# Kernel optimization log

Hardware: AMD Instinct MI355X
Metric: run time of the kernel (lower is better)

The kernel has to match this reference:

```python
import jax, jax.numpy as jnp
import numpy as np

B, T, E, H = 2, 2048, 1024, 4
Dk = E // H          # 256 head qk dim
Dv = Dk * 2          # 512 head v dim (expansion_ratio=2)
EPS = 1e-5
ROPE_BASE = 10000.0


def setup_inputs() -> dict:
    key = jax.random.key(0)
    ks = jax.random.split(key, 7)
    s = 0.02  # small init matching xavier gains in reset_parameters
    return {
        "x": jax.random.normal(ks[0], (B, T, E), jnp.float32),
        "Wq": jax.random.normal(ks[1], (E, E), jnp.float32) * s,
        "Wk": jax.random.normal(ks[2], (E, E), jnp.float32) * s,
        "Wv": jax.random.normal(ks[3], (E, 2 * E), jnp.float32) * s,
        "Wg": jax.random.normal(ks[4], (E, 2 * E), jnp.float32) * s,
        "Wo": jax.random.normal(ks[5], (2 * E, E), jnp.float32) * s,
        "gn_weight": jnp.ones((Dv,), jnp.float32),
    }


def _rotary(q, k):
    # q,k: [b, t, h, d]; non-interleaved (GPT-NeoX) rotary over the full head dim
    d = q.shape[-1]
    inv_freq = 1.0 / (ROPE_BASE ** (jnp.arange(0, d, 2, dtype=jnp.float32) / d))
    t = jnp.arange(q.shape[1], dtype=jnp.float32)
    freqs = jnp.einsum('t,f->tf', t, inv_freq)      # [t, d/2]
    cos = jnp.cos(freqs)[None, :, None, :]
    sin = jnp.sin(freqs)[None, :, None, :]

    def rot(x):
        x1, x2 = x[..., : d // 2], x[..., d // 2:]
        return jnp.concatenate([x1 * cos - x2 * sin, x2 * cos + x1 * sin], axis=-1)

    return rot(q), rot(k)


def reference(x, Wq, Wk, Wv, Wg, Wo, gn_weight):
    b, t, e = x.shape
    q = (x @ Wq).reshape(b, t, H, Dk)
    k = (x @ Wk).reshape(b, t, H, Dk)
    q, k = _rotary(q, k)
    q = q.transpose(0, 2, 1, 3) * (Dk ** -0.5)      # [b,h,t,dk], scale = head_qk_dim^-0.5
    k = k.transpose(0, 2, 1, 3)
    v = (x @ Wv).reshape(b, t, H, Dv).transpose(0, 2, 1, 3)  # [b,h,t,dv]

    # RetNet per-head decay: gamma_h = 1 - 2^-(5+h)
    gamma = 1.0 - jnp.exp2(-5.0 - jnp.arange(H, dtype=jnp.float32))
    ti = jnp.arange(t)
    n = ti[:, None] - ti[None, :]                   # t - s
    decay = jnp.where(
        n >= 0,
        gamma[:, None, None] ** jnp.maximum(n, 0).astype(jnp.float32),
        0.0,
    )                                               # [h,t,t] causal decayed mask

    scores = jnp.einsum('bhtd,bhsd->bhts', q, k) * decay[None]
    o = jnp.einsum('bhts,bhsd->bhtd', scores, v)    # [b,h,t,dv]
    o = o.transpose(0, 2, 1, 3)                     # [b,t,h,dv]

    # per-head RMSNorm (group_norm over head_v_dim)
    rms = jnp.sqrt(jnp.mean(o * o, axis=-1, keepdims=True) + EPS)
    o = o / rms * gn_weight

    # NOTE: the given source multiplies by raw g_proj(x) (gate_fn not applied in forward)
    g = x @ Wg                                      # [b,t,2E]
    return (o.reshape(b, t, H * Dv) * g) @ Wo       # [b,t,E]
```

## Files before the change

### kernel.cpp

```cpp
#include <hip/hip_runtime.h>
#include <hip/hip_bf16.h>

#define B_ 2
#define T_ 2048
#define E_ 1024
#define DK 256
#define DV 512
#define MROWS 4096
#define LDQKVG 6144
#define CHK 128
#define NCHK 16

typedef __attribute__((ext_vector_type(8))) short short8;
typedef __attribute__((ext_vector_type(4))) short short4v;
typedef __attribute__((ext_vector_type(4))) float floatx4;

typedef __attribute__((address_space(3))) unsigned as3_u32;
typedef const __attribute__((address_space(1))) unsigned as1_u32;

static __device__ __forceinline__ void gld_lds16(const unsigned short* gsrc, unsigned short* ldst) {
  __builtin_amdgcn_global_load_lds((as1_u32*)gsrc, (as3_u32*)ldst, 16, 0, 0);
}

static __device__ __forceinline__ float bf2f(unsigned short u) {
  union { unsigned int i; float f; } x; x.i = ((unsigned int)u) << 16; return x.f;
}
static __device__ __forceinline__ unsigned short f2bf(float f) {
  __hip_bfloat16 h = __float2bfloat16(f);
  return __builtin_bit_cast(unsigned short, h);
}
static __device__ __forceinline__ float load_as_f(const float* p) { return *p; }
static __device__ __forceinline__ float load_as_f(const unsigned short* p) { return bf2f(*p); }

__global__ void __launch_bounds__(256) convx_kernel(const float* __restrict__ x,
                                                    unsigned short* __restrict__ xb) {
  int i = blockIdx.x * 256 + threadIdx.x;
  size_t base = (size_t)i * 8;
  float4 a = *(const float4*)(x + base);
  float4 b = *(const float4*)(x + base + 4);
  short8 o;
  o[0] = (short)f2bf(a.x); o[1] = (short)f2bf(a.y);
  o[2] = (short)f2bf(a.z); o[3] = (short)f2bf(a.w);
  o[4] = (short)f2bf(b.x); o[5] = (short)f2bf(b.y);
  o[6] = (short)f2bf(b.z); o[7] = (short)f2bf(b.w);
  *(short8*)(xb + base) = o;
}

template<typename TIN>
__global__ void __launch_bounds__(256) transpose_bf16_kernel(
    const TIN* __restrict__ in, int ldin, unsigned short* __restrict__ out, int ldout) {
  __shared__ float tile[32][33];
  int c0 = blockIdx.x * 32, r0 = blockIdx.y * 32;
  int tx = threadIdx.x & 31, ty = threadIdx.x >> 5;
#pragma unroll
  for (int i = 0; i < 32; i += 8)
    tile[ty + i][tx] = load_as_f(&in[(size_t)(r0 + ty + i) * ldin + c0 + tx]);
  __syncthreads();
#pragma unroll
  for (int i = 0; i < 32; i += 8)
    out[(size_t)(c0 + ty + i) * ldout + r0 + tx] = f2bf(tile[tx][ty + i]);
}

__global__ void __launch_bounds__(256) transpose_weights_kernel(
    const float* __restrict__ Wq, const float* __restrict__ Wk,
    const float* __restrict__ Wv, const float* __restrict__ Wg,
    unsigned short* __restrict__ out) {
  __shared__ float tile[32][33];
  int bid = blockIdx.x;
  const float* in; unsigned short* o; int ldin, nbx;
  if (bid < 1024)      { in = Wq; o = out;                       ldin = 1024; nbx = 32; }
  else if (bid < 2048) { in = Wk; o = out + (size_t)1024 * 1024; ldin = 1024; nbx = 32; bid -= 1024; }
  else if (bid < 4096) { in = Wv; o = out + (size_t)2048 * 1024; ldin = 2048; nbx = 64; bid -= 2048; }
  else                 { in = Wg; o = out + (size_t)4096 * 1024; ldin = 2048; nbx = 64; bid -= 4096; }
  int c0 = (bid % nbx) * 32, r0 = (bid / nbx) * 32;
  int tx = threadIdx.x & 31, ty = threadIdx.x >> 5;
#pragma unroll
  for (int i = 0; i < 32; i += 8)
    tile[ty + i][tx] = in[(size_t)(r0 + ty + i) * ldin + c0 + tx];
  __syncthreads();
#pragma unroll
  for (int i = 0; i < 32; i += 8)
    o[(size_t)(c0 + ty + i) * 1024 + r0 + tx] = f2bf(tile[tx][ty + i]);
}

__global__ void __launch_bounds__(256) kts_transpose_kernel(
    const unsigned short* __restrict__ in, unsigned short* __restrict__ out) {
  __shared__ float tile[32][33];
  int c0 = blockIdx.x * 32, r0 = blockIdx.y * 32;
  int tx = threadIdx.x & 31, ty = threadIdx.x >> 5;
#pragma unroll
  for (int i = 0; i < 32; i += 8)
    tile[ty + i][tx] = bf2f(in[(size_t)(r0 + ty + i) * LDQKVG + c0 + tx]);
  __syncthreads();
  int h = c0 >> 8;
  float lg = log2f(1.0f - exp2f(-5.0f - (float)h));
  int t = r0 + tx;
  float fac = exp2f((float)(CHK - (t & (CHK - 1))) * lg);
#pragma unroll
  for (int i = 0; i < 32; i += 8)
    out[(size_t)(c0 + ty + i) * MROWS + r0 + tx] = f2bf(tile[tx][ty + i] * fac);
}

template<int BM, int BN, int WM_W, int WN_W, int MINW, bool F32OUT>
__global__ void __launch_bounds__(WM_W * WN_W * 64, MINW) gemmp_kernel(
    const unsigned short* __restrict__ A, int lda,
    const unsigned short* __restrict__ Bt, int ldb, int K,
    void* __restrict__ Cp, int ldc, int ccol0, int nbx) {
  constexpr int WAVES = WM_W * WN_W;
  constexpr int AG = BM / 16 / WAVES;
  constexpr int BG = BN / 16 / WAVES;
  constexpr int RM = BM / WM_W;
  constexpr int CN = BN / WN_W;
  constexpr int MB = RM / 16, NB = CN / 16;
  __shared__ __align__(16) unsigned short lds[3][(BM + BN) * 32];
  const int tid = threadIdx.x;
  const int lane = tid & 63;
  const int wid = tid >> 6;
  const int wm = wid / WN_W, wn = wid % WN_W;
  const int q8 = gridDim.x >> 3;
  const int bid = (blockIdx.x & 7) * q8 + (blockIdx.x >> 3);
  const int m0 = (bid % nbx) * BM;
  const int n0 = (bid / nbx) * BN;
  const unsigned short* Ab = A + (size_t)m0 * lda;
  const unsigned short* Bb = Bt + (size_t)n0 * ldb;
  const int NT = K / 32;

  auto stage = [&](int sl, int t) {
    const int k0 = t * 32;
#pragma unroll
    for (int j = 0; j < AG; ++j) {
      int g = wid * AG + j;
      int ci = g * 64 + lane;
      int row = ci >> 2, c = ci & 3;
      int cs = c ^ ((row >> 1) & 3);
      gld_lds16(Ab + (size_t)row * lda + k0 + cs * 8, &lds[sl][g * 512]);
    }
#pragma unroll
    for (int j = 0; j < BG; ++j) {
      int g = wid * BG + j;
      int ci = g * 64 + lane;
      int row = ci >> 2, c = ci & 3;
      int cs = c ^ ((row >> 1) & 3);
      gld_lds16(Bb + (size_t)row * ldb + k0 + cs * 8, &lds[sl][BM * 32 + g * 512]);
    }
  };

  floatx4 acc[MB][NB];
#pragma unroll
  for (int i = 0; i < MB; i++)
#pragma unroll
    for (int j = 0; j < NB; j++)
      acc[i][j] = (floatx4){0.f, 0.f, 0.f, 0.f};

  stage(0, 0);
  stage(1, 1);

  int cur = 0;
#pragma unroll 1
  for (int t = 0; t < NT; ++t) {
    if (t + 1 < NT) {
      if constexpr (AG + BG == 2) asm volatile("s_waitcnt vmcnt(2)" ::: "memory");
      else if constexpr (AG + BG == 3) asm volatile("s_waitcnt vmcnt(3)" ::: "memory");
      else if constexpr (AG + BG == 4) asm volatile("s_waitcnt vmcnt(4)" ::: "memory");
      else if constexpr (AG + BG == 6) asm volatile("s_waitcnt vmcnt(6)" ::: "memory");
      else asm volatile("s_waitcnt vmcnt(8)" ::: "memory");
    } else {
      asm volatile("s_waitcnt vmcnt(0)" ::: "memory");
    }
    __builtin_amdgcn_s_barrier();
    asm volatile("" ::: "memory");
    int sl = cur + 2; if (sl >= 3) sl -= 3;
    if (t + 2 < NT) stage(sl, t + 2);

    const unsigned short* As_ = lds[cur];
    const unsigned short* Bs_ = lds[cur] + BM * 32;
    short8 af[MB], bfv[NB];
#pragma unroll
    for (int i = 0; i < MB; ++i) {
      int row = wm * RM + i * 16 + (lane & 15);
      af[i] = *(const short8*)&As_[row * 32 + (((lane >> 4) ^ ((row >> 1) & 3)) * 8)];
    }
#pragma unroll
    for (int j = 0; j < NB; ++j) {
      int nn = wn * CN + j * 16 + (lane & 15);
      bfv[j] = *(const short8*)&Bs_[nn * 32 + (((lane >> 4) ^ ((nn >> 1) & 3)) * 8)];
    }
#pragma unroll
    for (int i = 0; i < MB; ++i)
#pragma unroll
      for (int j = 0; j < NB; ++j)
        acc[i][j] = __builtin_amdgcn_mfma_f32_16x16x32_bf16(af[i], bfv[j], acc[i][j], 0, 0, 0);
    cur = cur + 1 == 3 ? 0 : cur + 1;
  }

#pragma unroll
  for (int i = 0; i < MB; ++i)
#pragma unroll
    for (int j = 0; j < NB; ++j)
#pragma unroll
      for (int r = 0; r < 4; ++r) {
        int row = m0 + wm * RM + i * 16 + (lane >> 4) * 4 + r;
        int col = ccol0 + n0 + wn * CN + j * 16 + (lane & 15);
        float v = acc[i][j][r];
        if (F32OUT) ((float*)Cp)[(size_t)row * ldc + col] = v;
        else ((unsigned short*)Cp)[(size_t)row * ldc + col] = f2bf(v);
      }
}

__global__ void __launch_bounds__(256) rope_kernel(unsigned short* __restrict__ qkvg) {
  int idx = blockIdx.x * 256 + threadIdx.x;
  int j = idx & 127;
  int h = (idx >> 7) & 3;
  int row = idx >> 9;
  int t = row & (T_ - 1);
  float invf = exp2f(-(float)j * (13.287712379549449f / 128.0f));
  float ang = (float)t * invf;
  float c = cosf(ang), s = sinf(ang);
  float lg = log2f(1.0f - exp2f(-5.0f - (float)h));
  float sq = 0.0625f * exp2f((float)(t & (CHK - 1)) * lg);
  size_t base = (size_t)row * LDQKVG + h * DK + j;
  float q1 = bf2f(qkvg[base]), q2 = bf2f(qkvg[base + 128]);
  float k1 = bf2f(qkvg[base + E_]), k2 = bf2f(qkvg[base + E_ + 128]);
  qkvg[base]            = f2bf((q1 * c - q2 * s) * sq);
  qkvg[base + 128]      = f2bf((q2 * c + q1 * s) * sq);
  qkvg[base + E_]       = f2bf(k1 * c - k2 * s);
  qkvg[base + E_ + 128] = f2bf(k2 * c + k1 * s);
}

__global__ void __launch_bounds__(256) state_kernel(
    const unsigned short* __restrict__ kTs, const unsigned short* __restrict__ vT,
    unsigned short* __restrict__ Sbuf) {
  const int lane = threadIdx.x & 63, wid = threadIdx.x >> 6;
  const int bh = blockIdx.x & 7, dkt = (blockIdx.x >> 3) & 3, dvt = (blockIdx.x >> 5) & 15;
  const int b = bh >> 2, h = bh & 3;
  const float lg = log2f(1.0f - exp2f(-5.0f - (float)h));
  const float g128 = exp2f((float)CHK * lg);
  const int dk0 = dkt * 64 + wid * 16;
  const int dv0 = dvt * 32;
  const unsigned short* arow = kTs + (size_t)(h * DK + dk0 + (lane & 15)) * MROWS + b * T_ + (lane >> 4) * 8;
  const unsigned short* brow = vT + (size_t)(h * DV + dv0 + (lane & 15)) * MROWS + b * T_ + (lane >> 4) * 8;
  floatx4 acc[2];
  acc[0] = (floatx4){0.f, 0.f, 0.f, 0.f};
  acc[1] = (floatx4){0.f, 0.f, 0.f, 0.f};
#pragma unroll 1
  for (int c = 0; c < NCHK; ++c) {
    size_t sb = (size_t)(c * 8 + bh) * (DV * DK);
#pragma unroll
    for (int nb = 0; nb < 2; ++nb) {
      short4v o;
#pragma unroll
      for (int r = 0; r < 4; ++r) o[r] = (short)f2bf(acc[nb][r]);
      *(short4v*)&Sbuf[sb + (size_t)(dv0 + nb * 16 + (lane & 15)) * DK + dk0 + (lane >> 4) * 4] = o;
    }
#pragma unroll
    for (int nb = 0; nb < 2; ++nb)
#pragma unroll
      for (int r = 0; r < 4; ++r) acc[nb][r] *= g128;
#pragma unroll
    for (int ks = 0; ks < 4; ++ks) {
      short8 a = *(const short8*)(arow + c * CHK + ks * 32);
#pragma unroll
      for (int nb = 0; nb < 2; ++nb) {
        short8 bb = *(const short8*)(brow + (size_t)nb * 16 * MROWS + c * CHK + ks * 32);
        acc[nb] = __builtin_amdgcn_mfma_f32_16x16x32_bf16(a, bb, acc[nb], 0, 0, 0);
      }
    }
  }
}

__global__ void __launch_bounds__(256) retention2_kernel(
    const unsigned short* __restrict__ qkvg, const unsigned short* __restrict__ vT,
    const unsigned short* __restrict__ Sbuf, const float* __restrict__ gnw,
    unsigned short* __restrict__ og, float* __restrict__ ssbuf) {
  __shared__ unsigned short k_lds[2][32 * 256];
  __shared__ unsigned short v_lds[2][256 * 32];
  __shared__ unsigned short s_lds[4][16 * 40];
  const int tid = threadIdx.x, lane = tid & 63, wid = tid >> 6;
  const int bh  = blockIdx.x & 7;
  const int c   = (blockIdx.x >> 3) & 15;
  const int dvh = (blockIdx.x >> 7) & 1;
  const int rhf = (blockIdx.x >> 8) & 1;
  const int b = bh >> 2, h = bh & 3;
  const float lg = log2f(1.0f - exp2f(-5.0f - (float)h));
  const int rb0 = b * T_ + c * CHK + rhf * 64;
  const int taub = rhf * 64 + wid * 16;
  const int nst = rhf ? 4 : 2;
  const unsigned short* kbase = qkvg + (size_t)(b * T_ + c * CHK) * LDQKVG + E_ + h * DK;
  const unsigned short* vbase = vT + (size_t)(h * DV + dvh * 256) * MROWS + b * T_ + c * CHK;
  const unsigned short* Sp = Sbuf + (size_t)(c * 8 + bh) * (DV * DK) + (size_t)dvh * 256 * DK;

  auto stage = [&](int buf, int st) {
    int s0 = st * 32;
#pragma unroll
    for (int j = 0; j < 4; ++j) {
      int ci = (wid * 4 + j) * 64 + lane;
      int row = ci >> 5, cc = ci & 31;
      int cs = cc ^ (row & 7);
      gld_lds16(kbase + (size_t)(s0 + row) * LDQKVG + cs * 8, &k_lds[buf][(wid * 4 + j) * 512]);
    }
#pragma unroll
    for (int j = 0; j < 4; ++j) {
      int ci = (wid * 4 + j) * 64 + lane;
      int dv = ci >> 2, cc = ci & 3;
      int cs = cc ^ ((dv ^ (dv >> 2)) & 3);
      gld_lds16(vbase + (size_t)dv * MROWS + s0 + cs * 8, &v_lds[buf][(wid * 4 + j) * 512]);
    }
  };

  stage(0, 0);

  short8 qf[8];
  {
    int qrow = rb0 + wid * 16 + (lane & 15);
    const unsigned short* qp = qkvg + (size_t)qrow * LDQKVG + h * DK + (lane >> 4) * 8;
#pragma unroll
    for (int kk = 0; kk < 8; kk++) qf[kk] = *(const short8*)(qp + kk * 32);
  }
  floatx4 oacc[16];
#pragma unroll
  for (int nb = 0; nb < 16; ++nb) oacc[nb] = (floatx4){0.f, 0.f, 0.f, 0.f};
#pragma unroll
  for (int ks = 0; ks < 8; ++ks) {
#pragma unroll
    for (int nb = 0; nb < 16; ++nb) {
      short8 sf = *(const short8*)&Sp[(size_t)(nb * 16 + (lane & 15)) * DK + ks * 32 + (lane >> 4) * 8];
      oacc[nb] = __builtin_amdgcn_mfma_f32_16x16x32_bf16(qf[ks], sf, oacc[nb], 0, 0, 0);
    }
  }

#pragma unroll 1
  for (int st = 0; st < nst; ++st) {
    const int cur = st & 1;
    __syncthreads();
    if (st + 1 < nst) stage(cur ^ 1, st + 1);
#pragma unroll
    for (int ch = 0; ch < 2; ++ch) {
      floatx4 f = (floatx4){0.f, 0.f, 0.f, 0.f};
      const int srow = ch * 16 + (lane & 15);
#pragma unroll
      for (int kk = 0; kk < 8; kk++) {
        int cc = (kk * 4 + (lane >> 4)) ^ (srow & 7);
        short8 kf = *(const short8*)&k_lds[cur][srow * 256 + cc * 8];
        f = __builtin_amdgcn_mfma_f32_16x16x32_bf16(qf[kk], kf, f, 0, 0, 0);
      }
#pragma unroll
      for (int r = 0; r < 4; ++r) {
        int lr = (lane >> 4) * 4 + r;
        int sig = st * 32 + ch * 16 + (lane & 15);
        int n = taub + lr - sig;
        float val = (n >= 0) ? f[r] * exp2f(-(float)sig * lg) : 0.0f;
        s_lds[wid][lr * 40 + ch * 16 + (lane & 15)] = f2bf(val);
      }
    }
    short8 af = *(const short8*)&s_lds[wid][(lane & 15) * 40 + (lane >> 4) * 8];
#pragma unroll
    for (int nb = 0; nb < 16; ++nb) {
      int dv = nb * 16 + (lane & 15);
      int cc = (lane >> 4) ^ ((dv ^ (dv >> 2)) & 3);
      short8 vf = *(const short8*)&v_lds[cur][dv * 32 + cc * 8];
      oacc[nb] = __builtin_amdgcn_mfma_f32_16x16x32_bf16(af, vf, oacc[nb], 0, 0, 0);
    }
  }
#pragma unroll
  for (int r = 0; r < 4; ++r) {
    float ss = 0.f;
#pragma unroll
    for (int nb = 0; nb < 16; nb++) { float xv = oacc[nb][r]; ss += xv * xv; }
    ss += __shfl_xor(ss, 1, 64);
    ss += __shfl_xor(ss, 2, 64);
    ss += __shfl_xor(ss, 4, 64);
    ss += __shfl_xor(ss, 8, 64);
    if ((lane & 15) == 0) {
      int row = rb0 + wid * 16 + (lane >> 4) * 4 + r;
      ssbuf[(size_t)row * 8 + h * 2 + dvh] = ss;
    }
  }
#pragma unroll
  for (int r = 0; r < 4; ++r) {
    int row = rb0 + wid * 16 + (lane >> 4) * 4 + r;
    size_t growbase = (size_t)row * LDQKVG + 4096 + h * DV + dvh * 256;
    size_t orowbase = (size_t)row * LDQKVG + h * DV + dvh * 256;
#pragma unroll
    for (int nb = 0; nb < 16; nb++) {
      int col = nb * 16 + (lane & 15);
      float gv = bf2f(qkvg[growbase + col]);
      og[orowbase + col] = f2bf(oacc[nb][r] * gnw[dvh * 256 + col] * gv);
    }
  }
}

__global__ void __launch_bounds__(256) normalize_kernel(
    unsigned short* __restrict__ og, const float* __restrict__ ssbuf) {
  int i = blockIdx.x * 256 + threadIdx.x;
  size_t e0 = (size_t)i * 8;
  int row = (int)(e0 >> 11);
  int col = (int)(e0 & 2047);
  int h = col >> 9;
  float ss = ssbuf[(size_t)row * 8 + h * 2] + ssbuf[(size_t)row * 8 + h * 2 + 1];
  float inv = rsqrtf(ss * (1.0f / 512.0f) + 1e-5f);
  size_t a = (size_t)row * LDQKVG + col;
  short8 v = *(const short8*)(og + a);
#pragma unroll
  for (int j = 0; j < 8; j++) v[j] = (short)f2bf(bf2f((unsigned short)v[j]) * inv);
  *(short8*)(og + a) = v;
}

extern "C" void kernel_launch(void* const* d_in, const int* in_sizes, int n_in,
                              void* d_out, int out_size, void* d_ws, size_t ws_size,
                              hipStream_t stream) {
  const float* x   = (const float*)d_in[0];
  const float* Wq  = (const float*)d_in[1];
  const float* Wk  = (const float*)d_in[2];
  const float* Wv  = (const float*)d_in[3];
  const float* Wg  = (const float*)d_in[4];
  const float* Wo  = (const float*)d_in[5];
  const float* gnw = (const float*)d_in[6];
  float* out = (float*)d_out;

  char* ws = (char*)d_ws;
  size_t off = 0;
  auto alloc = [&](size_t bytes) { char* p = ws + off; off += (bytes + 255) & ~(size_t)255; return p; };
  unsigned short* qkvg = (unsigned short*)alloc((size_t)MROWS * LDQKVG * 2);
  unsigned short* vT   = (unsigned short*)alloc((size_t)2048 * MROWS * 2);
  char* regS = alloc((size_t)NCHK * 8 * DV * DK * 2);
  unsigned short* Sbuf  = (unsigned short*)regS;
  unsigned short* xb    = (unsigned short*)regS;
  unsigned short* WallT = (unsigned short*)(regS + 8388608);
  char* regK = alloc((size_t)1024 * MROWS * 2);
  unsigned short* kTs = (unsigned short*)regK;
  unsigned short* WoT = (unsigned short*)regK;
  float* ssbuf = (float*)alloc((size_t)MROWS * 8 * 4);
  unsigned short* og = qkvg + 2048;

  convx_kernel<<<2048, 256, 0, stream>>>(x, xb);

  transpose_weights_kernel<<<6144, 256, 0, stream>>>(Wq, Wk, Wv, Wg, WallT);

  gemmp_kernel<128, 256, 1, 4, 2, false><<<768, 256, 0, stream>>>(
      xb, 1024, WallT, 1024, 1024, qkvg, LDQKVG, 0, 32);

  rope_kernel<<<8192, 256, 0, stream>>>(qkvg);

  kts_transpose_kernel<<<dim3(32, 128), 256, 0, stream>>>(qkvg + E_, kTs);

  transpose_bf16_kernel<unsigned short><<<dim3(64, 128), 256, 0, stream>>>(qkvg + 2048, LDQKVG, vT, MROWS);

  state_kernel<<<512, 256, 0, stream>>>(kTs, vT, Sbuf);

  transpose_bf16_kernel<float><<<dim3(32, 64), 256, 0, stream>>>(Wo, 1024, WoT, 2048);

  retention2_kernel<<<512, 256, 0, stream>>>(qkvg, vT, Sbuf, gnw, og, ssbuf);

  normalize_kernel<<<4096, 256, 0, stream>>>(og, ssbuf);

  gemmp_kernel<128, 128, 2, 2, 3, true><<<256, 256, 0, stream>>>(
      og, LDQKVG, WoT, 2048, 2048, out, E_, 0, 32);
}
```

Baseline: 226.8 us.

## Precompute RoPE table, vectorize rope kernel, retune QKVG GEMM and state loop

Splits RoPE into a kernel that precomputes a cos/sin table and a rope pass that loads and stores 8 bf16 values per thread with 16-byte accesses, so there are fewer threads, fewer transcendental calls and wider memory transactions. The QKVG projection GEMM changes its template configuration and launches 512 threads per block. The state kernel's chunk loop is now unrolled by 4. The table shares workspace memory with kTs/WoT, which is safe only because those buffers are written after rope runs, and it adds one small launch.

```diff
diff --git a/kernel.cpp b/kernel.cpp
--- a/kernel.cpp
+++ b/kernel.cpp
@@ -207,24 +207,43 @@
       }
 }
 
-__global__ void __launch_bounds__(256) rope_kernel(unsigned short* __restrict__ qkvg) {
+__global__ void __launch_bounds__(256) rope_table_kernel(float2* __restrict__ tab) {
   int idx = blockIdx.x * 256 + threadIdx.x;
-  int j = idx & 127;
-  int h = (idx >> 7) & 3;
-  int row = idx >> 9;
-  int t = row & (T_ - 1);
+  int t = idx >> 7, j = idx & 127;
   float invf = exp2f(-(float)j * (13.287712379549449f / 128.0f));
   float ang = (float)t * invf;
-  float c = cosf(ang), s = sinf(ang);
+  tab[idx] = make_float2(cosf(ang), sinf(ang));
+}
+
+__global__ void __launch_bounds__(256) rope_kernel(unsigned short* __restrict__ qkvg,
+                                                   const float2* __restrict__ tab) {
+  int idx = blockIdx.x * 256 + threadIdx.x;
+  int jv = idx & 15;
+  int h = (idx >> 4) & 3;
+  int row = idx >> 6;
+  int t = row & (T_ - 1);
+  int j0 = jv * 8;
   float lg = log2f(1.0f - exp2f(-5.0f - (float)h));
   float sq = 0.0625f * exp2f((float)(t & (CHK - 1)) * lg);
-  size_t base = (size_t)row * LDQKVG + h * DK + j;
-  float q1 = bf2f(qkvg[base]), q2 = bf2f(qkvg[base + 128]);
-  float k1 = bf2f(qkvg[base + E_]), k2 = bf2f(qkvg[base + E_ + 128]);
-  qkvg[base]            = f2bf((q1 * c - q2 * s) * sq);
-  qkvg[base + 128]      = f2bf((q2 * c + q1 * s) * sq);
-  qkvg[base + E_]       = f2bf(k1 * c - k2 * s);
-  qkvg[base + E_ + 128] = f2bf(k2 * c + k1 * s);
+  size_t base = (size_t)row * LDQKVG + h * DK + j0;
+  short8 q1 = *(const short8*)&qkvg[base],      q2 = *(const short8*)&qkvg[base + 128];
+  short8 k1 = *(const short8*)&qkvg[base + E_], k2 = *(const short8*)&qkvg[base + E_ + 128];
+  short8 oq1, oq2, ok1, ok2;
+#pragma unroll
+  for (int e = 0; e < 8; ++e) {
+    float2 cs = tab[(t << 7) + j0 + e];
+    float c = cs.x, s = cs.y;
+    float a1 = bf2f((unsigned short)q1[e]), a2 = bf2f((unsigned short)q2[e]);
+    float b1 = bf2f((unsigned short)k1[e]), b2 = bf2f((unsigned short)k2[e]);
+    oq1[e] = (short)f2bf((a1 * c - a2 * s) * sq);
+    oq2[e] = (short)f2bf((a2 * c + a1 * s) * sq);
+    ok1[e] = (short)f2bf(b1 * c - b2 * s);
+    ok2[e] = (short)f2bf(b2 * c + b1 * s);
+  }
+  *(short8*)&qkvg[base]            = oq1;
+  *(short8*)&qkvg[base + 128]      = oq2;
+  *(short8*)&qkvg[base + E_]       = ok1;
+  *(short8*)&qkvg[base + E_ + 128] = ok2;
 }
 
 __global__ void __launch_bounds__(256) state_kernel(
@@ -242,7 +261,7 @@
   floatx4 acc[2];
   acc[0] = (floatx4){0.f, 0.f, 0.f, 0.f};
   acc[1] = (floatx4){0.f, 0.f, 0.f, 0.f};
-#pragma unroll 1
+#pragma unroll 4
   for (int c = 0; c < NCHK; ++c) {
     size_t sb = (size_t)(c * 8 + bh) * (DV * DK);
 #pragma unroll
@@ -429,6 +448,7 @@
   char* regK = alloc((size_t)1024 * MROWS * 2);
   unsigned short* kTs = (unsigned short*)regK;
   unsigned short* WoT = (unsigned short*)regK;
+  float2* ropetab = (float2*)regK;
   float* ssbuf = (float*)alloc((size_t)MROWS * 8 * 4);
   unsigned short* og = qkvg + 2048;
 
@@ -436,10 +456,12 @@
 
   transpose_weights_kernel<<<6144, 256, 0, stream>>>(Wq, Wk, Wv, Wg, WallT);
 
-  gemmp_kernel<128, 256, 1, 4, 2, false><<<768, 256, 0, stream>>>(
+  rope_table_kernel<<<1024, 256, 0, stream>>>(ropetab);
+
+  gemmp_kernel<128, 256, 2, 4, 4, false><<<768, 512, 0, stream>>>(
       xb, 1024, WallT, 1024, 1024, qkvg, LDQKVG, 0, 32);
 
-  rope_kernel<<<8192, 256, 0, stream>>>(qkvg);
+  rope_kernel<<<1024, 256, 0, stream>>>(qkvg, ropetab);
 
   kts_transpose_kernel<<<dim3(32, 128), 256, 0, stream>>>(qkvg + E_, kTs);
 
```

Measured after the change: 227.6 us. About the same (+0.3%).
